# Kernel tuning notes

Hardware: AMD Instinct MI355X
Metric: run time of the kernel (lower is better)

## Reference

```python
import jax, jax.numpy as jnp
import numpy as np

B, V, C, D, H, W = 2, 3, 32, 48, 128, 160


def _bilinear_sample(img, x, y):
    # img: [C,H,W]; x,y: [N] pixel coords; zero padding outside the image
    Ci, Hi, Wi = img.shape
    x0 = jnp.floor(x); y0 = jnp.floor(y)
    x1 = x0 + 1.0; y1 = y0 + 1.0
    wx1 = x - x0; wx0 = 1.0 - wx1
    wy1 = y - y0; wy0 = 1.0 - wy1

    def gather(xi, yi):
        valid = (xi >= 0) & (xi <= Wi - 1) & (yi >= 0) & (yi <= Hi - 1)
        xc = jnp.clip(xi, 0, Wi - 1).astype(jnp.int32)
        yc = jnp.clip(yi, 0, Hi - 1).astype(jnp.int32)
        return img[:, yc, xc] * valid.astype(img.dtype)  # [C,N]

    return (gather(x0, y0) * (wx0 * wy0) + gather(x1, y0) * (wx1 * wy0)
            + gather(x0, y1) * (wx0 * wy1) + gather(x1, y1) * (wx1 * wy1))


def homo_warping(src_fea, src_proj, ref_proj, depth_values):
    # src_fea [B,C,H,W], projs [B,4,4], depth_values [B,D] -> [B,C,D,H,W]
    Bn, Cn, Hn, Wn = src_fea.shape
    Dn = depth_values.shape[1]
    proj = src_proj @ jnp.linalg.inv(ref_proj)          # [B,4,4]
    rot = proj[:, :3, :3]
    trans = proj[:, :3, 3]
    ys, xs = jnp.meshgrid(jnp.arange(Hn, dtype=src_fea.dtype),
                          jnp.arange(Wn, dtype=src_fea.dtype), indexing='ij')
    xyz = jnp.stack([xs.ravel(), ys.ravel(), jnp.ones(Hn * Wn, src_fea.dtype)])  # [3,HW]
    rot_xyz = jnp.einsum('bij,jn->bin', rot, xyz)       # [B,3,HW]
    pts = rot_xyz[:, :, None, :] * depth_values[:, None, :, None] \
          + trans[:, :, None, None]                     # [B,3,D,HW]
    z = pts[:, 2]
    z = jnp.where(jnp.abs(z) < 1e-6, 1e-6, z)
    px = (pts[:, 0] / z).reshape(Bn, -1)                # [B,D*HW]
    py = (pts[:, 1] / z).reshape(Bn, -1)
    warped = jax.vmap(_bilinear_sample)(src_fea, px, py)  # [B,C,D*HW]
    return warped.reshape(Bn, Cn, Dn, Hn, Wn)


def setup_inputs():
    key = jax.random.key(0)
    k1, k2 = jax.random.split(key)
    features = jax.random.normal(k1, (V, B, C, H, W), jnp.float32)
    # realistic pinhole projection matrices K @ [R|t] (4x4)
    f = 300.0
    K = np.array([[f, 0, W / 2, 0], [0, f, H / 2, 0],
                  [0, 0, 1, 0], [0, 0, 0, 1]], np.float32)
    projs = []
    for v in range(V):
        E = np.eye(4, dtype=np.float32)
        E[0, 3] = 2.0 * v   # small camera baseline
        E[1, 3] = -1.0 * v
        projs.append(K @ E)
    proj_matrices = jnp.asarray(np.broadcast_to(np.stack(projs), (B, V, 4, 4)).copy())
    depth_values = jnp.tile(jnp.linspace(425.0, 935.0, D, dtype=jnp.float32)[None], (B, 1))
    reg_w = jax.random.normal(k2, (1, C, 3, 3, 3), jnp.float32) * 0.05
    reg_b = jnp.zeros((1,), jnp.float32)
    return {"features": features, "proj_matrices": proj_matrices,
            "depth_values": depth_values, "num_depth": D,
            "reg_w": reg_w, "reg_b": reg_b}


def reference(features, proj_matrices, depth_values, num_depth, reg_w, reg_b):
    num_views = features.shape[0]
    ref_feature = features[0]                         # [B,C,H,W]
    ref_proj = proj_matrices[:, 0]
    Bn, Cn, Hn, Wn = ref_feature.shape
    ref_volume = jnp.broadcast_to(ref_feature[:, :, None], (Bn, Cn, num_depth, Hn, Wn))
    volume_sum = ref_volume
    volume_sq_sum = ref_volume ** 2
    for v in range(1, num_views):
        wv = homo_warping(features[v], proj_matrices[:, v], ref_proj, depth_values)
        volume_sum = volume_sum + wv
        volume_sq_sum = volume_sq_sum + wv * wv
    variance = volume_sq_sum / num_views - (volume_sum / num_views) ** 2
    # cost regularization: Conv3d(C->1, k=3, pad=1)
    cost = jax.lax.conv_general_dilated(
        variance, reg_w, (1, 1, 1), [(1, 1), (1, 1), (1, 1)],
        dimension_numbers=('NCDHW', 'OIDHW', 'NCDHW'))
    cost = cost + reg_b[None, :, None, None, None]
    prob = jax.nn.softmax(cost[:, 0], axis=1)         # [B,D,H,W]
    depth = jnp.sum(prob * depth_values[:, :, None, None], axis=1)  # [B,H,W]
    # photometric confidence: sum over 4 consecutive depth probs (== 4*avg_pool3d)
    psum4 = jax.lax.reduce_window(prob, 0.0, jax.lax.add, (1, 4, 1, 1), (1, 1, 1, 1),
                                  [(0, 0), (1, 2), (0, 0), (0, 0)])
    didx = jnp.sum(prob * jnp.arange(num_depth, dtype=prob.dtype)[None, :, None, None], axis=1)
    didx = jnp.clip(didx.astype(jnp.int32), 0, num_depth - 1)
    conf = jnp.take_along_axis(psum4, didx[:, None], axis=1)[:, 0]
    return depth, conf
```

## Files before the change

### kernel.cpp

```cpp
#include <hip/hip_runtime.h>
#include <hip/hip_bf16.h>
#include <hip/hip_fp16.h>

#define Hh 128
#define Ww 160
#define Cc 32
#define Dd 48
#define Bb 2
#define Vv 3
#define HW (Hh*Ww)
#define VS 32

typedef _Float16 f16x8 __attribute__((ext_vector_type(8)));
typedef float f32x4 __attribute__((ext_vector_type(4)));

__global__ void k_transpose(const float* __restrict__ f, const float* __restrict__ pm,
                            const float* __restrict__ wt, ushort* __restrict__ featT,
                            float* __restrict__ P, ushort* __restrict__ Bfr) {
    __shared__ float t[Cc][Ww + 1];
    const int tid = threadIdx.x;
    if (blockIdx.x == 0 && tid < 64) {
        if (tid < Bb * (Vv - 1)) {
            int b = tid >> 1;
            int v = (tid & 1) + 1;
            const float* ref = pm + (b * Vv + 0) * 16;
            const float* src = pm + (b * Vv + v) * 16;
            float A[4][8];
            for (int i = 0; i < 4; ++i)
                for (int j = 0; j < 4; ++j) {
                    A[i][j] = ref[i * 4 + j];
                    A[i][4 + j] = (i == j) ? 1.0f : 0.0f;
                }
            for (int col = 0; col < 4; ++col) {
                int piv = col;
                for (int r = col + 1; r < 4; ++r)
                    if (fabsf(A[r][col]) > fabsf(A[piv][col])) piv = r;
                if (piv != col)
                    for (int j = 0; j < 8; ++j) { float tmp = A[col][j]; A[col][j] = A[piv][j]; A[piv][j] = tmp; }
                float inv = 1.0f / A[col][col];
                for (int j = 0; j < 8; ++j) A[col][j] *= inv;
                for (int r = 0; r < 4; ++r) {
                    if (r == col) continue;
                    float fct = A[r][col];
                    for (int j = 0; j < 8; ++j) A[r][j] -= fct * A[col][j];
                }
            }
            float Pm[3][4];
            for (int i = 0; i < 3; ++i)
                for (int j = 0; j < 4; ++j) {
                    float s = 0.f;
                    for (int k = 0; k < 4; ++k) s += src[i * 4 + k] * A[k][4 + j];
                    Pm[i][j] = s;
                }
            float* o = P + tid * 12;
            o[0] = Pm[0][0]; o[1] = Pm[0][1]; o[2] = Pm[0][2];
            o[3] = Pm[1][0]; o[4] = Pm[1][1]; o[5] = Pm[1][2];
            o[6] = Pm[2][0]; o[7] = Pm[2][1]; o[8] = Pm[2][2];
            o[9] = Pm[0][3]; o[10] = Pm[1][3]; o[11] = Pm[2][3];
        }
        int kd = tid & 15, q = tid >> 4;
        for (int tap = 0; tap < 9; ++tap) {
            ushort* dst = Bfr + (tap * 64 + tid) * 8;
            for (int j = 0; j < 8; ++j) {
                float w = (kd < 3) ? wt[(q * 8 + j) * 27 + kd * 9 + tap] : 0.f;
                __half h = __float2half(w);
                dst[j] = *(ushort*)&h;
            }
        }
    }
    int slice = blockIdx.x;
    int vb = slice / Hh, y = slice % Hh;
    const float* src = f + (size_t)vb * Cc * HW + (size_t)y * Ww;
    ushort* dst = featT + ((size_t)vb * Hh + y) * Ww * Cc;
    for (int i = tid; i < Cc * (Ww / 4); i += 256) {
        int c = i / (Ww / 4), x4 = (i - c * (Ww / 4)) * 4;
        float4 v = *(const float4*)(src + (size_t)c * HW + x4);
        t[c][x4] = v.x; t[c][x4 + 1] = v.y; t[c][x4 + 2] = v.z; t[c][x4 + 3] = v.w;
    }
    __syncthreads();
    for (int i = tid; i < Ww * 4; i += 256) {
        int x = i >> 2, c8 = i & 3;
        union { uint4 u; ushort s[8]; } pk;
#pragma unroll
        for (int j = 0; j < 8; ++j) {
            __half h = __float2half(t[c8 * 8 + j][x]);
            pk.s[j] = *(ushort*)&h;
        }
        *(uint4*)&dst[x * Cc + c8 * 8] = pk.u;
    }
}

__global__ __launch_bounds__(256, 4)
void k_main(const ushort* __restrict__ featT, const float* __restrict__ P,
            const float* __restrict__ dvals, const ushort* __restrict__ Bfr,
            ushort* __restrict__ S) {
    __shared__ ushort vsh[324 * VS];
    __shared__ unsigned int offs[324 * 8];
    __shared__ unsigned int wgts[324 * 4];
    __shared__ float rt[24];
    const int tid = threadIdx.x;
    const int b = blockIdx.z, d = blockIdx.y;
    const int tileY = blockIdx.x / 10, tileX = blockIdx.x - (blockIdx.x / 10) * 10;

    if (tid < 24) rt[tid] = P[b * 24 + tid];
    const float depth = dvals[b * Dd + d];
    __syncthreads();

#pragma unroll 1
    for (int p = tid; p < 324; p += 256) {
        int pyt = p / 18, pxt = p - pyt * 18;
        int gy = tileY * 16 + pyt - 1, gx = tileX * 16 + pxt - 1;
        if ((unsigned)gy >= (unsigned)Hh || (unsigned)gx >= (unsigned)Ww) continue;
#pragma unroll
        for (int vi = 0; vi < 2; ++vi) {
            const float* M = &rt[vi * 12];
            float fgx = (float)gx, fgy = (float)gy;
            float rx = M[0] * fgx + M[1] * fgy + M[2];
            float ry = M[3] * fgx + M[4] * fgy + M[5];
            float rz = M[6] * fgx + M[7] * fgy + M[8];
            float X = rx * depth + M[9];
            float Y = ry * depth + M[10];
            float Z = rz * depth + M[11];
            float z = (fabsf(Z) < 1e-6f) ? 1e-6f : Z;
            float u = X / z, vv = Y / z;
            float x0f = floorf(u), y0f = floorf(vv);
            float fx = u - x0f, fy = vv - y0f;
            int x0 = (int)x0f, y0 = (int)y0f;
            int x1 = x0 + 1, y1 = y0 + 1;
            bool vx0 = (x0 >= 0) && (x0 <= Ww - 1);
            bool vx1 = (x1 >= 0) && (x1 <= Ww - 1);
            bool vy0 = (y0 >= 0) && (y0 <= Hh - 1);
            bool vy1 = (y1 >= 0) && (y1 <= Hh - 1);
            int xc0 = min(max(x0, 0), Ww - 1), xc1 = min(max(x1, 0), Ww - 1);
            int yc0 = min(max(y0, 0), Hh - 1), yc1 = min(max(y1, 0), Hh - 1);
            unsigned int p00 = (unsigned)(yc0 * Ww + xc0);
            unsigned int p01 = (unsigned)(yc0 * Ww + xc1);
            unsigned int p10 = (unsigned)(yc1 * Ww + xc0);
            unsigned int p11 = (unsigned)(yc1 * Ww + xc1);
            float w0 = (vx0 && vy0) ? (1.f - fx) * (1.f - fy) : 0.f;
            float w1 = (vx1 && vy0) ? fx * (1.f - fy) : 0.f;
            float w2 = (vx0 && vy1) ? (1.f - fx) * fy : 0.f;
            float w3 = (vx1 && vy1) ? fx * fy : 0.f;
            unsigned int* od = &offs[p * 8 + vi * 4];
            od[0] = p00 << 6;
            od[1] = p01 << 6;
            od[2] = p10 << 6;
            od[3] = p11 << 6;
            __half2 ha = __floats2half2_rn(w0, w1);
            __half2 hb = __floats2half2_rn(w2, w3);
            wgts[p * 4 + vi * 2 + 0] = *(unsigned int*)&ha;
            wgts[p * 4 + vi * 2 + 1] = *(unsigned int*)&hb;
        }
    }
    __syncthreads();

    const ushort* b1 = featT + (size_t)(1 * Bb + b) * HW * Cc;
    const ushort* b2 = featT + (size_t)(2 * Bb + b) * HW * Cc;
    const ushort* br = featT + (size_t)b * HW * Cc;

#pragma unroll 1
    for (int i = tid; i < 1296; i += 256) {
        int p = i >> 2, q = i & 3;
        int pyt = p / 18, pxt = p - pyt * 18;
        int gy = tileY * 16 + pyt - 1, gx = tileX * 16 + pxt - 1;
        ushort* dst = &vsh[p * VS + ((q ^ (p & 3)) << 3)];
        if ((unsigned)gy >= (unsigned)Hh || (unsigned)gx >= (unsigned)Ww) {
            *(uint4*)dst = make_uint4(0u, 0u, 0u, 0u);
            continue;
        }
        const unsigned int qb = (unsigned)(q << 4);
        const uint4 o1 = *(const uint4*)&offs[p * 8];
        const uint4 o2 = *(const uint4*)&offs[p * 8 + 4];
        const uint4 wwp = *(const uint4*)&wgts[p * 4];
        __half2 hv0 = *(__half2*)&wwp.x;
        __half2 hv1 = *(__half2*)&wwp.y;
        __half2 hv2 = *(__half2*)&wwp.z;
        __half2 hv3 = *(__half2*)&wwp.w;
        __half2 w00 = __half2half2(__low2half(hv0)), w01 = __half2half2(__high2half(hv0));
        __half2 w02 = __half2half2(__low2half(hv1)), w03 = __half2half2(__high2half(hv1));
        __half2 w10 = __half2half2(__low2half(hv2)), w11 = __half2half2(__high2half(hv2));
        __half2 w12 = __half2half2(__low2half(hv3)), w13 = __half2half2(__high2half(hv3));
        const __half2 third2 = __float2half2_rn(1.0f / 3.0f);
        union U { uint4 u; __half2 h[4]; };
        U R_, C0, C1, C2, C3, E0, E1, E2, E3, V;
        R_.u = *(const uint4*)((const char*)br + ((unsigned)((gy * Ww + gx) << 6) + qb));
        C0.u = *(const uint4*)((const char*)b1 + (o1.x + qb));
        C1.u = *(const uint4*)((const char*)b1 + (o1.y + qb));
        C2.u = *(const uint4*)((const char*)b1 + (o1.z + qb));
        C3.u = *(const uint4*)((const char*)b1 + (o1.w + qb));
        E0.u = *(const uint4*)((const char*)b2 + (o2.x + qb));
        E1.u = *(const uint4*)((const char*)b2 + (o2.y + qb));
        E2.u = *(const uint4*)((const char*)b2 + (o2.z + qb));
        E3.u = *(const uint4*)((const char*)b2 + (o2.w + qb));
#pragma unroll
        for (int k = 0; k < 4; ++k) {
            __half2 s1 = __hmul2(w00, C0.h[k]);
            s1 = __hfma2(w01, C1.h[k], s1);
            s1 = __hfma2(w02, C2.h[k], s1);
            s1 = __hfma2(w03, C3.h[k], s1);
            __half2 s2 = __hmul2(w10, E0.h[k]);
            s2 = __hfma2(w11, E1.h[k], s2);
            s2 = __hfma2(w12, E2.h[k], s2);
            s2 = __hfma2(w13, E3.h[k], s2);
            __half2 r = R_.h[k];
            __half2 sum = __hadd2(__hadd2(r, s1), s2);
            __half2 sq = __hmul2(r, r);
            sq = __hfma2(s1, s1, sq);
            sq = __hfma2(s2, s2, sq);
            __half2 m = __hmul2(sum, third2);
            __half2 var = __hfma2(__hneg2(m), m, __hmul2(sq, third2));
            V.h[k] = var;
        }
        *(uint4*)dst = V.u;
    }
    __syncthreads();

    const int lane = tid & 63;
    const int wave = tid >> 6;
    const int q = lane >> 4;
    const int n = lane & 15;
    uint4 bf[9];
#pragma unroll
    for (int tap = 0; tap < 9; ++tap)
        bf[tap] = *(const uint4*)(Bfr + ((tap * 64 + lane) << 3));
#pragma unroll 1
    for (int rr = 0; rr < 4; ++rr) {
        int row = wave * 4 + rr;
        f32x4 acc = {0.f, 0.f, 0.f, 0.f};
#pragma unroll
        for (int tap = 0; tap < 9; ++tap) {
            int kh = tap / 3, kw = tap - 3 * (tap / 3);
            int slot = (row + kh) * 18 + n + kw;
            union { uint4 u; f16x8 v; } A, Bf;
            A.u  = *(const uint4*)&vsh[slot * VS + (q ^ (slot & 3)) * 8];
            Bf.u = bf[tap];
            acc = __builtin_amdgcn_mfma_f32_16x16x32_f16(A.v, Bf.v, acc, 0, 0, 0);
        }
        if (n < 3) {
            int gy = tileY * 16 + row;
            int gxb = tileX * 16 + q * 4;
            union { uint2 u; ushort s[4]; } pk;
#pragma unroll
            for (int j = 0; j < 4; ++j) {
                __half h = __float2half(acc[j]);
                pk.s[j] = *(ushort*)&h;
            }
            *(uint2*)&S[((size_t)(b * 3 + n) * Dd + d) * HW + (size_t)gy * Ww + gxb] = pk.u;
        }
    }
}

__global__ __launch_bounds__(256)
void k_post(const ushort* __restrict__ S, const float* __restrict__ dvals,
            float* __restrict__ out) {
    const int tid = threadIdx.x;
    const int lane = tid & 63, wave = tid >> 6;
    const int q = lane >> 4;
    const int pl = lane & 15;
    int gid = ((blockIdx.x * 4 + wave) * 16 + pl) * 2;
    int b = gid / HW;
    int pix = gid - b * HW;
    const ushort* S0 = S + ((size_t)(b * 3 + 0) * Dd) * HW + pix;
    const ushort* S1 = S + ((size_t)(b * 3 + 1) * Dd) * HW + pix;
    const ushort* S2 = S + ((size_t)(b * 3 + 2) * Dd) * HW + pix;
    const int d0 = q * 12;
    float2 cost[12];
#pragma unroll
    for (int j = 0; j < 12; ++j) {
        int dd = d0 + j;
        float2 c = __half22float2(*(const __half2*)&S1[(size_t)dd * HW]);
        if (dd > 0) {
            float2 a = __half22float2(*(const __half2*)&S0[(size_t)(dd - 1) * HW]);
            c.x += a.x; c.y += a.y;
        }
        if (dd < Dd - 1) {
            float2 a = __half22float2(*(const __half2*)&S2[(size_t)(dd + 1) * HW]);
            c.x += a.x; c.y += a.y;
        }
        cost[j] = c;
    }
    float mx = cost[0].x, my = cost[0].y;
#pragma unroll
    for (int j = 1; j < 12; ++j) { mx = fmaxf(mx, cost[j].x); my = fmaxf(my, cost[j].y); }
    mx = fmaxf(mx, __shfl_xor(mx, 16)); mx = fmaxf(mx, __shfl_xor(mx, 32));
    my = fmaxf(my, __shfl_xor(my, 16)); my = fmaxf(my, __shfl_xor(my, 32));
    float sx = 0.f, sy = 0.f, depx = 0.f, depy = 0.f, dix = 0.f, diy = 0.f;
#pragma unroll
    for (int j = 0; j < 12; ++j) {
        float dv = dvals[b * Dd + d0 + j];
        float fd = (float)(d0 + j);
        float ex = __expf(cost[j].x - mx);
        float ey = __expf(cost[j].y - my);
        cost[j].x = ex; cost[j].y = ey;
        sx += ex; sy += ey;
        depx += ex * dv; depy += ey * dv;
        dix += ex * fd;  diy += ey * fd;
    }
    sx += __shfl_xor(sx, 16); sx += __shfl_xor(sx, 32);
    sy += __shfl_xor(sy, 16); sy += __shfl_xor(sy, 32);
    depx += __shfl_xor(depx, 16); depx += __shfl_xor(depx, 32);
    depy += __shfl_xor(depy, 16); depy += __shfl_xor(depy, 32);
    dix += __shfl_xor(dix, 16); dix += __shfl_xor(dix, 32);
    diy += __shfl_xor(diy, 16); diy += __shfl_xor(diy, 32);
    float invx = 1.0f / sx, invy = 1.0f / sy;
    int didx = min(max((int)(dix * invx), 0), Dd - 1);
    int didy = min(max((int)(diy * invy), 0), Dd - 1);
    float wx = 0.f, wy = 0.f;
#pragma unroll
    for (int j = 0; j < 12; ++j) {
        int dd = d0 + j;
        wx += ((dd >= didx - 1) && (dd <= didx + 2)) ? cost[j].x : 0.f;
        wy += ((dd >= didy - 1) && (dd <= didy + 2)) ? cost[j].y : 0.f;
    }
    wx += __shfl_xor(wx, 16); wx += __shfl_xor(wx, 32);
    wy += __shfl_xor(wy, 16); wy += __shfl_xor(wy, 32);
    if (q == 0) {
        *(float2*)&out[gid] = make_float2(depx * invx, depy * invy);
        *(float2*)&out[Bb * HW + gid] = make_float2(wx * invx, wy * invy);
    }
}

extern "C" void kernel_launch(void* const* d_in, const int* in_sizes, int n_in,
                              void* d_out, int out_size, void* d_ws, size_t ws_size,
                              hipStream_t stream) {
    const float* features = (const float*)d_in[0];
    const float* pm       = (const float*)d_in[1];
    const float* dvals    = (const float*)d_in[2];
    const float* reg_w    = (const float*)d_in[4];
    float* outp = (float*)d_out;

    char* ws = (char*)d_ws;
    ushort* featT = (ushort*)ws;
    size_t featT_bytes = (size_t)Vv * Bb * Hh * Ww * Cc * sizeof(ushort);
    float* P = (float*)(ws + featT_bytes);
    ushort* S = (ushort*)(ws + featT_bytes + 512);
    size_t S_bytes = (size_t)Bb * 3 * Dd * HW * sizeof(ushort);
    ushort* Bfr = (ushort*)(ws + featT_bytes + 512 + S_bytes);

    k_transpose<<<Vv * Bb * Hh, 256, 0, stream>>>(features, pm, reg_w, featT, P, Bfr);
    k_main<<<dim3(80, Dd, Bb), 256, 0, stream>>>(featT, P, dvals, Bfr, S);
    k_post<<<(Bb * HW) / 128, 256, 0, stream>>>(S, dvals, outp);
}
```

Measured before the change: 153.5 us.

## Fuse variance into MFMA: apply per-tap channel weights then spatially sum in LDS

```diff
diff --git a/kernel.cpp b/kernel.cpp
--- a/kernel.cpp
+++ b/kernel.cpp
@@ -9,7 +9,7 @@
 #define Bb 2
 #define Vv 3
 #define HW (Hh*Ww)
-#define VS 32
+#define TSTRIDE 340
 
 typedef _Float16 f16x8 __attribute__((ext_vector_type(8)));
 typedef float f32x4 __attribute__((ext_vector_type(4)));
@@ -58,13 +58,16 @@
             o[6] = Pm[2][0]; o[7] = Pm[2][1]; o[8] = Pm[2][2];
             o[9] = Pm[0][3]; o[10] = Pm[1][3]; o[11] = Pm[2][3];
         }
-        int kd = tid & 15, q = tid >> 4;
-        for (int tap = 0; tap < 9; ++tap) {
-            ushort* dst = Bfr + (tap * 64 + tid) * 8;
-            for (int j = 0; j < 8; ++j) {
-                float w = (kd < 3) ? wt[(q * 8 + j) * 27 + kd * 9 + tap] : 0.f;
+        int j16 = tid & 15, q = tid >> 4;
+        for (int m = 0; m < 3; ++m) {
+            ushort* dst = Bfr + (m * 64 + tid) * 8;
+            int j = m * 16 + j16;
+            int tap = j >> 2, kd = j & 3;
+            bool valid = (tap < 9) && (kd < 3);
+            for (int e = 0; e < 8; ++e) {
+                float w = valid ? wt[(q * 8 + e) * 27 + kd * 9 + tap] : 0.f;
                 __half h = __float2half(w);
-                dst[j] = *(ushort*)&h;
+                dst[e] = *(ushort*)&h;
             }
         }
     }
@@ -94,9 +97,9 @@
 void k_main(const ushort* __restrict__ featT, const float* __restrict__ P,
             const float* __restrict__ dvals, const ushort* __restrict__ Bfr,
             ushort* __restrict__ S) {
-    __shared__ ushort vsh[324 * VS];
-    __shared__ unsigned int offs[324 * 8];
+    __shared__ unsigned int offs[324 * 4];
     __shared__ unsigned int wgts[324 * 4];
+    __shared__ ushort t2[36 * TSTRIDE];
     __shared__ float rt[24];
     const int tid = threadIdx.x;
     const int b = blockIdx.z, d = blockIdx.y;
@@ -141,11 +144,8 @@
             float w1 = (vx1 && vy0) ? fx * (1.f - fy) : 0.f;
             float w2 = (vx0 && vy1) ? (1.f - fx) * fy : 0.f;
             float w3 = (vx1 && vy1) ? fx * fy : 0.f;
-            unsigned int* od = &offs[p * 8 + vi * 4];
-            od[0] = p00 << 6;
-            od[1] = p01 << 6;
-            od[2] = p10 << 6;
-            od[3] = p11 << 6;
+            offs[p * 4 + vi * 2 + 0] = p00 | (p01 << 16);
+            offs[p * 4 + vi * 2 + 1] = p10 | (p11 << 16);
             __half2 ha = __floats2half2_rn(w0, w1);
             __half2 hb = __floats2half2_rn(w2, w3);
             wgts[p * 4 + vi * 2 + 0] = *(unsigned int*)&ha;
@@ -158,95 +158,122 @@
     const ushort* b2 = featT + (size_t)(2 * Bb + b) * HW * Cc;
     const ushort* br = featT + (size_t)b * HW * Cc;
 
-#pragma unroll 1
-    for (int i = tid; i < 1296; i += 256) {
-        int p = i >> 2, q = i & 3;
-        int pyt = p / 18, pxt = p - pyt * 18;
-        int gy = tileY * 16 + pyt - 1, gx = tileX * 16 + pxt - 1;
-        ushort* dst = &vsh[p * VS + ((q ^ (p & 3)) << 3)];
-        if ((unsigned)gy >= (unsigned)Hh || (unsigned)gx >= (unsigned)Ww) {
-            *(uint4*)dst = make_uint4(0u, 0u, 0u, 0u);
-            continue;
-        }
-        const unsigned int qb = (unsigned)(q << 4);
-        const uint4 o1 = *(const uint4*)&offs[p * 8];
-        const uint4 o2 = *(const uint4*)&offs[p * 8 + 4];
-        const uint4 wwp = *(const uint4*)&wgts[p * 4];
-        __half2 hv0 = *(__half2*)&wwp.x;
-        __half2 hv1 = *(__half2*)&wwp.y;
-        __half2 hv2 = *(__half2*)&wwp.z;
-        __half2 hv3 = *(__half2*)&wwp.w;
-        __half2 w00 = __half2half2(__low2half(hv0)), w01 = __half2half2(__high2half(hv0));
-        __half2 w02 = __half2half2(__low2half(hv1)), w03 = __half2half2(__high2half(hv1));
-        __half2 w10 = __half2half2(__low2half(hv2)), w11 = __half2half2(__high2half(hv2));
-        __half2 w12 = __half2half2(__low2half(hv3)), w13 = __half2half2(__high2half(hv3));
-        const __half2 third2 = __float2half2_rn(1.0f / 3.0f);
-        union U { uint4 u; __half2 h[4]; };
-        U R_, C0, C1, C2, C3, E0, E1, E2, E3, V;
-        R_.u = *(const uint4*)((const char*)br + ((unsigned)((gy * Ww + gx) << 6) + qb));
-        C0.u = *(const uint4*)((const char*)b1 + (o1.x + qb));
-        C1.u = *(const uint4*)((const char*)b1 + (o1.y + qb));
-        C2.u = *(const uint4*)((const char*)b1 + (o1.z + qb));
-        C3.u = *(const uint4*)((const char*)b1 + (o1.w + qb));
-        E0.u = *(const uint4*)((const char*)b2 + (o2.x + qb));
-        E1.u = *(const uint4*)((const char*)b2 + (o2.y + qb));
-        E2.u = *(const uint4*)((const char*)b2 + (o2.z + qb));
-        E3.u = *(const uint4*)((const char*)b2 + (o2.w + qb));
-#pragma unroll
-        for (int k = 0; k < 4; ++k) {
-            __half2 s1 = __hmul2(w00, C0.h[k]);
-            s1 = __hfma2(w01, C1.h[k], s1);
-            s1 = __hfma2(w02, C2.h[k], s1);
-            s1 = __hfma2(w03, C3.h[k], s1);
-            __half2 s2 = __hmul2(w10, E0.h[k]);
-            s2 = __hfma2(w11, E1.h[k], s2);
-            s2 = __hfma2(w12, E2.h[k], s2);
-            s2 = __hfma2(w13, E3.h[k], s2);
-            __half2 r = R_.h[k];
-            __half2 sum = __hadd2(__hadd2(r, s1), s2);
-            __half2 sq = __hmul2(r, r);
-            sq = __hfma2(s1, s1, sq);
-            sq = __hfma2(s2, s2, sq);
-            __half2 m = __hmul2(sum, third2);
-            __half2 var = __hfma2(__hneg2(m), m, __hmul2(sq, third2));
-            V.h[k] = var;
-        }
-        *(uint4*)dst = V.u;
-    }
-    __syncthreads();
-
     const int lane = tid & 63;
     const int wave = tid >> 6;
     const int q = lane >> 4;
     const int n = lane & 15;
-    uint4 bf[9];
-#pragma unroll
-    for (int tap = 0; tap < 9; ++tap)
-        bf[tap] = *(const uint4*)(Bfr + ((tap * 64 + lane) << 3));
+
+    union F { uint4 u; __half2 h[4]; f16x8 v; };
+    F Bf0, Bf1, Bf2;
+    Bf0.u = *(const uint4*)(Bfr + (0 * 64 + lane) * 8);
+    Bf1.u = *(const uint4*)(Bfr + (1 * 64 + lane) * 8);
+    Bf2.u = *(const uint4*)(Bfr + (2 * 64 + lane) * 8);
+
 #pragma unroll 1
-    for (int rr = 0; rr < 4; ++rr) {
-        int row = wave * 4 + rr;
-        f32x4 acc = {0.f, 0.f, 0.f, 0.f};
-#pragma unroll
-        for (int tap = 0; tap < 9; ++tap) {
-            int kh = tap / 3, kw = tap - 3 * (tap / 3);
-            int slot = (row + kh) * 18 + n + kw;
-            union { uint4 u; f16x8 v; } A, Bf;
-            A.u  = *(const uint4*)&vsh[slot * VS + (q ^ (slot & 3)) * 8];
-            Bf.u = bf[tap];
-            acc = __builtin_amdgcn_mfma_f32_16x16x32_f16(A.v, Bf.v, acc, 0, 0, 0);
-        }
-        if (n < 3) {
-            int gy = tileY * 16 + row;
-            int gxb = tileX * 16 + q * 4;
-            union { uint2 u; ushort s[4]; } pk;
-#pragma unroll
-            for (int j = 0; j < 4; ++j) {
-                __half h = __float2half(acc[j]);
-                pk.s[j] = *(ushort*)&h;
+    for (int g = wave; g < 21; g += 4) {
+        int slot = g * 16 + n;
+        int p = (slot < 324) ? slot : 323;
+        int pyt = p / 18, pxt = p - pyt * 18;
+        int gy = tileY * 16 + pyt - 1, gx = tileX * 16 + pxt - 1;
+        bool live = (slot < 324) && ((unsigned)gy < (unsigned)Hh) && ((unsigned)gx < (unsigned)Ww);
+        F V;
+        V.u = make_uint4(0u, 0u, 0u, 0u);
+        if (live) {
+            const unsigned qb = (unsigned)(q << 4);
+            uint4 oo = *(const uint4*)&offs[p * 4];
+            uint4 wwp = *(const uint4*)&wgts[p * 4];
+            const char* b1c = (const char*)b1 + qb;
+            const char* b2c = (const char*)b2 + qb;
+            unsigned o00 = (oo.x & 0xffffu) << 6;
+            unsigned o01 = (oo.x >> 16) << 6;
+            unsigned o10 = (oo.y & 0xffffu) << 6;
+            unsigned o11 = (oo.y >> 16) << 6;
+            unsigned o20 = (oo.z & 0xffffu) << 6;
+            unsigned o21 = (oo.z >> 16) << 6;
+            unsigned o30 = (oo.w & 0xffffu) << 6;
+            unsigned o31 = (oo.w >> 16) << 6;
+            __half2 hv0 = *(__half2*)&wwp.x;
+            __half2 hv1 = *(__half2*)&wwp.y;
+            __half2 hv2 = *(__half2*)&wwp.z;
+            __half2 hv3 = *(__half2*)&wwp.w;
+            __half2 w00 = __half2half2(__low2half(hv0)), w01 = __half2half2(__high2half(hv0));
+            __half2 w02 = __half2half2(__low2half(hv1)), w03 = __half2half2(__high2half(hv1));
+            __half2 w10 = __half2half2(__low2half(hv2)), w11 = __half2half2(__high2half(hv2));
+            __half2 w12 = __half2half2(__low2half(hv3)), w13 = __half2half2(__high2half(hv3));
+            const __half2 third2 = __float2half2_rn(1.0f / 3.0f);
+            F R_, C0, C1, C2, C3, E0, E1, E2, E3;
+            R_.u = *(const uint4*)((const char*)br + (((unsigned)(gy * Ww + gx)) << 6) + qb);
+            C0.u = *(const uint4*)(b1c + o00);
+            C1.u = *(const uint4*)(b1c + o01);
+            C2.u = *(const uint4*)(b1c + o10);
+            C3.u = *(const uint4*)(b1c + o11);
+            E0.u = *(const uint4*)(b2c + o20);
+            E1.u = *(const uint4*)(b2c + o21);
+            E2.u = *(const uint4*)(b2c + o30);
+            E3.u = *(const uint4*)(b2c + o31);
+#pragma unroll
+            for (int k = 0; k < 4; ++k) {
+                __half2 s1 = __hmul2(w00, C0.h[k]);
+                s1 = __hfma2(w01, C1.h[k], s1);
+                s1 = __hfma2(w02, C2.h[k], s1);
+                s1 = __hfma2(w03, C3.h[k], s1);
+                __half2 s2 = __hmul2(w10, E0.h[k]);
+                s2 = __hfma2(w11, E1.h[k], s2);
+                s2 = __hfma2(w12, E2.h[k], s2);
+                s2 = __hfma2(w13, E3.h[k], s2);
+                __half2 r = R_.h[k];
+                __half2 sum = __hadd2(__hadd2(r, s1), s2);
+                __half2 sq = __hmul2(r, r);
+                sq = __hfma2(s1, s1, sq);
+                sq = __hfma2(s2, s2, sq);
+                __half2 m = __hmul2(sum, third2);
+                __half2 var = __hfma2(__hneg2(m), m, __hmul2(sq, third2));
+                V.h[k] = var;
             }
-            *(uint2*)&S[((size_t)(b * 3 + n) * Dd + d) * HW + (size_t)gy * Ww + gxb] = pk.u;
-        }
+        }
+        f32x4 a0 = {0.f, 0.f, 0.f, 0.f};
+        f32x4 a1 = {0.f, 0.f, 0.f, 0.f};
+        f32x4 a2 = {0.f, 0.f, 0.f, 0.f};
+        a0 = __builtin_amdgcn_mfma_f32_16x16x32_f16(V.v, Bf0.v, a0, 0, 0, 0);
+        a1 = __builtin_amdgcn_mfma_f32_16x16x32_f16(V.v, Bf1.v, a1, 0, 0, 0);
+        a2 = __builtin_amdgcn_mfma_f32_16x16x32_f16(V.v, Bf2.v, a2, 0, 0, 0);
+        int sb = g * 16 + q * 4;
+        union { uint2 u; ushort s[4]; } pk;
+#pragma unroll
+        for (int r = 0; r < 4; ++r) { __half h = __float2half(a0[r]); pk.s[r] = *(ushort*)&h; }
+        *(uint2*)&t2[(0 * 16 + n) * TSTRIDE + sb] = pk.u;
+#pragma unroll
+        for (int r = 0; r < 4; ++r) { __half h = __float2half(a1[r]); pk.s[r] = *(ushort*)&h; }
+        *(uint2*)&t2[(16 + n) * TSTRIDE + sb] = pk.u;
+        if (n < 4) {
+#pragma unroll
+            for (int r = 0; r < 4; ++r) { __half h = __float2half(a2[r]); pk.s[r] = *(ushort*)&h; }
+            *(uint2*)&t2[(32 + n) * TSTRIDE + sb] = pk.u;
+        }
+    }
+    __syncthreads();
+
+    {
+        int x = tid & 15, y = tid >> 4;
+        float s0 = 0.f, s1 = 0.f, s2 = 0.f;
+#pragma unroll
+        for (int ky = 0; ky < 3; ++ky) {
+#pragma unroll
+            for (int kx = 0; kx < 3; ++kx) {
+                int tap = ky * 3 + kx;
+                int sl = (y + ky) * 18 + (x + kx);
+                const ushort* tp = &t2[(tap * 4) * TSTRIDE + sl];
+                s0 += __half2float(*(const __half*)&tp[0]);
+                s1 += __half2float(*(const __half*)&tp[TSTRIDE]);
+                s2 += __half2float(*(const __half*)&tp[2 * TSTRIDE]);
+            }
+        }
+        int gy = tileY * 16 + y, gx = tileX * 16 + x;
+        size_t base = (size_t)gy * Ww + gx;
+        __half h0 = __float2half(s0), h1 = __float2half(s1), h2 = __float2half(s2);
+        S[((size_t)(b * 3 + 0) * Dd + d) * HW + base] = *(ushort*)&h0;
+        S[((size_t)(b * 3 + 1) * Dd + d) * HW + base] = *(ushort*)&h1;
+        S[((size_t)(b * 3 + 2) * Dd + d) * HW + base] = *(ushort*)&h2;
     }
 }
 
```

Result: slower. 170.2 us (+10.9%).

## Stage source-view bounding windows in LDS and loop over depth chunks per block

Applied to the files above, without the earlier changes.

```diff
diff --git a/kernel.cpp b/kernel.cpp
--- a/kernel.cpp
+++ b/kernel.cpp
@@ -10,6 +10,9 @@
 #define Vv 3
 #define HW (Hh*Ww)
 #define VS 32
+#define WPX 336
+#define NSLOT 180
+#define DCH 16
 
 typedef _Float16 f16x8 __attribute__((ext_vector_type(8)));
 typedef float f32x4 __attribute__((ext_vector_type(4)));
@@ -90,67 +93,75 @@
     }
 }
 
-__global__ __launch_bounds__(256, 4)
+__global__ __launch_bounds__(256, 2)
 void k_main(const ushort* __restrict__ featT, const float* __restrict__ P,
             const float* __restrict__ dvals, const ushort* __restrict__ Bfr,
             ushort* __restrict__ S) {
-    __shared__ ushort vsh[324 * VS];
-    __shared__ unsigned int offs[324 * 8];
-    __shared__ unsigned int wgts[324 * 4];
+    __shared__ ushort win[2 * WPX * 32];
+    __shared__ ushort refw[NSLOT * 32];
+    __shared__ ushort vsh[NSLOT * VS];
+    __shared__ unsigned int offs[NSLOT * 4];
+    __shared__ unsigned int wgts[NSLOT * 4];
     __shared__ float rt[24];
+    __shared__ float uvz[2][8][3];
+    __shared__ int bb[8];
+    __shared__ int wok[2];
     const int tid = threadIdx.x;
-    const int b = blockIdx.z, d = blockIdx.y;
+    const int b = blockIdx.z;
+    const int cb = blockIdx.y * DCH;
     const int tileY = blockIdx.x / 10, tileX = blockIdx.x - (blockIdx.x / 10) * 10;
 
     if (tid < 24) rt[tid] = P[b * 24 + tid];
-    const float depth = dvals[b * Dd + d];
     __syncthreads();
 
-#pragma unroll 1
-    for (int p = tid; p < 324; p += 256) {
-        int pyt = p / 18, pxt = p - pyt * 18;
-        int gy = tileY * 16 + pyt - 1, gx = tileX * 16 + pxt - 1;
-        if ((unsigned)gy >= (unsigned)Hh || (unsigned)gx >= (unsigned)Ww) continue;
-#pragma unroll
-        for (int vi = 0; vi < 2; ++vi) {
-            const float* M = &rt[vi * 12];
-            float fgx = (float)gx, fgy = (float)gy;
-            float rx = M[0] * fgx + M[1] * fgy + M[2];
-            float ry = M[3] * fgx + M[4] * fgy + M[5];
-            float rz = M[6] * fgx + M[7] * fgy + M[8];
-            float X = rx * depth + M[9];
-            float Y = ry * depth + M[10];
-            float Z = rz * depth + M[11];
-            float z = (fabsf(Z) < 1e-6f) ? 1e-6f : Z;
-            float u = X / z, vv = Y / z;
-            float x0f = floorf(u), y0f = floorf(vv);
-            float fx = u - x0f, fy = vv - y0f;
-            int x0 = (int)x0f, y0 = (int)y0f;
-            int x1 = x0 + 1, y1 = y0 + 1;
-            bool vx0 = (x0 >= 0) && (x0 <= Ww - 1);
-            bool vx1 = (x1 >= 0) && (x1 <= Ww - 1);
-            bool vy0 = (y0 >= 0) && (y0 <= Hh - 1);
-            bool vy1 = (y1 >= 0) && (y1 <= Hh - 1);
-            int xc0 = min(max(x0, 0), Ww - 1), xc1 = min(max(x1, 0), Ww - 1);
-            int yc0 = min(max(y0, 0), Hh - 1), yc1 = min(max(y1, 0), Hh - 1);
-            unsigned int p00 = (unsigned)(yc0 * Ww + xc0);
-            unsigned int p01 = (unsigned)(yc0 * Ww + xc1);
-            unsigned int p10 = (unsigned)(yc1 * Ww + xc0);
-            unsigned int p11 = (unsigned)(yc1 * Ww + xc1);
-            float w0 = (vx0 && vy0) ? (1.f - fx) * (1.f - fy) : 0.f;
-            float w1 = (vx1 && vy0) ? fx * (1.f - fy) : 0.f;
-            float w2 = (vx0 && vy1) ? (1.f - fx) * fy : 0.f;
-            float w3 = (vx1 && vy1) ? fx * fy : 0.f;
-            unsigned int* od = &offs[p * 8 + vi * 4];
-            od[0] = p00 << 6;
-            od[1] = p01 << 6;
-            od[2] = p10 << 6;
-            od[3] = p11 << 6;
-            __half2 ha = __floats2half2_rn(w0, w1);
-            __half2 hb = __floats2half2_rn(w2, w3);
-            wgts[p * 4 + vi * 2 + 0] = *(unsigned int*)&ha;
-            wgts[p * 4 + vi * 2 + 1] = *(unsigned int*)&hb;
-        }
+    if (tid < 16) {
+        int vi = tid >> 3, s = tid & 7;
+        int corner = s & 3, de = s >> 2;
+        float dmn = 1e30f, dmx = -1e30f;
+        for (int k = 0; k < DCH; ++k) {
+            float dv = dvals[b * Dd + cb + k];
+            dmn = fminf(dmn, dv); dmx = fmaxf(dmx, dv);
+        }
+        float depth = de ? dmx : dmn;
+        float fgx = (float)(tileX * 16 + ((corner & 1) ? 16 : -1));
+        float fgy = (float)(tileY * 8 + ((corner & 2) ? 8 : -1));
+        const float* M = &rt[vi * 12];
+        float rx = M[0] * fgx + M[1] * fgy + M[2];
+        float ry = M[3] * fgx + M[4] * fgy + M[5];
+        float rz = M[6] * fgx + M[7] * fgy + M[8];
+        float X = rx * depth + M[9];
+        float Y = ry * depth + M[10];
+        float Z = rz * depth + M[11];
+        float z = (fabsf(Z) < 1e-6f) ? 1e-6f : Z;
+        uvz[vi][s][0] = X / z;
+        uvz[vi][s][1] = Y / z;
+        uvz[vi][s][2] = Z;
+    }
+    __syncthreads();
+    if (tid < 2) {
+        int vi = tid;
+        float umin = 1e30f, umax = -1e30f, vmin = 1e30f, vmax = -1e30f;
+        int npos = 0, nneg = 0;
+        for (int s = 0; s < 8; ++s) {
+            float u = uvz[vi][s][0], v = uvz[vi][s][1], z = uvz[vi][s][2];
+            npos += (z > 1e-5f); nneg += (z < -1e-5f);
+            umin = fminf(umin, u); umax = fmaxf(umax, u);
+            vmin = fminf(vmin, v); vmax = fmaxf(vmax, v);
+        }
+        bool ok = (npos == 8) || (nneg == 8);
+        ok = ok && (umin <= umax) && (vmin <= vmax);
+        umin = fmaxf(fminf(umin, 1e5f), -1e5f); umax = fmaxf(fminf(umax, 1e5f), -1e5f);
+        vmin = fmaxf(fminf(vmin, 1e5f), -1e5f); vmax = fmaxf(fminf(vmax, 1e5f), -1e5f);
+        int bx = max(0, (int)floorf(umin) - 1);
+        int ex = min(Ww - 1, (int)ceilf(umax) + 2);
+        int by = max(0, (int)floorf(vmin) - 1);
+        int ey = min(Hh - 1, (int)ceilf(vmax) + 2);
+        int ww2 = ex - bx + 1, wh2 = ey - by + 1;
+        ok = ok && (ww2 > 0) && (wh2 > 0) && (ww2 * wh2 <= WPX);
+        if (!ok) { bx = 0; by = 0; ww2 = 1; wh2 = 1; }
+        bb[vi * 4 + 0] = bx; bb[vi * 4 + 1] = by;
+        bb[vi * 4 + 2] = ww2; bb[vi * 4 + 3] = wh2;
+        wok[vi] = ok ? 1 : 0;
     }
     __syncthreads();
 
@@ -158,95 +169,205 @@
     const ushort* b2 = featT + (size_t)(2 * Bb + b) * HW * Cc;
     const ushort* br = featT + (size_t)b * HW * Cc;
 
-#pragma unroll 1
-    for (int i = tid; i < 1296; i += 256) {
-        int p = i >> 2, q = i & 3;
+#pragma unroll
+    for (int vi = 0; vi < 2; ++vi) {
+        if (!wok[vi]) continue;
+        int bx = bb[vi * 4 + 0], by = bb[vi * 4 + 1], ww2 = bb[vi * 4 + 2], wh2 = bb[vi * 4 + 3];
+        const ushort* src = vi ? b2 : b1;
+        ushort* wdst = win + vi * (WPX * 32);
+        int total = ww2 * wh2 * 4;
+        for (int i = tid; i < total; i += 256) {
+            int q = i & 3, w = i >> 2;
+            int wy = w / ww2, wx = w - wy * ww2;
+            *(uint4*)&wdst[(w << 5) + (q << 3)] =
+                *(const uint4*)&src[(size_t)((by + wy) * Ww + bx + wx) * Cc + (q << 3)];
+        }
+    }
+    for (int i = tid; i < NSLOT * 4; i += 256) {
+        int q = i & 3, p = i >> 2;
         int pyt = p / 18, pxt = p - pyt * 18;
-        int gy = tileY * 16 + pyt - 1, gx = tileX * 16 + pxt - 1;
-        ushort* dst = &vsh[p * VS + ((q ^ (p & 3)) << 3)];
-        if ((unsigned)gy >= (unsigned)Hh || (unsigned)gx >= (unsigned)Ww) {
-            *(uint4*)dst = make_uint4(0u, 0u, 0u, 0u);
-            continue;
-        }
-        const unsigned int qb = (unsigned)(q << 4);
-        const uint4 o1 = *(const uint4*)&offs[p * 8];
-        const uint4 o2 = *(const uint4*)&offs[p * 8 + 4];
-        const uint4 wwp = *(const uint4*)&wgts[p * 4];
-        __half2 hv0 = *(__half2*)&wwp.x;
-        __half2 hv1 = *(__half2*)&wwp.y;
-        __half2 hv2 = *(__half2*)&wwp.z;
-        __half2 hv3 = *(__half2*)&wwp.w;
-        __half2 w00 = __half2half2(__low2half(hv0)), w01 = __half2half2(__high2half(hv0));
-        __half2 w02 = __half2half2(__low2half(hv1)), w03 = __half2half2(__high2half(hv1));
-        __half2 w10 = __half2half2(__low2half(hv2)), w11 = __half2half2(__high2half(hv2));
-        __half2 w12 = __half2half2(__low2half(hv3)), w13 = __half2half2(__high2half(hv3));
-        const __half2 third2 = __float2half2_rn(1.0f / 3.0f);
-        union U { uint4 u; __half2 h[4]; };
-        U R_, C0, C1, C2, C3, E0, E1, E2, E3, V;
-        R_.u = *(const uint4*)((const char*)br + ((unsigned)((gy * Ww + gx) << 6) + qb));
-        C0.u = *(const uint4*)((const char*)b1 + (o1.x + qb));
-        C1.u = *(const uint4*)((const char*)b1 + (o1.y + qb));
-        C2.u = *(const uint4*)((const char*)b1 + (o1.z + qb));
-        C3.u = *(const uint4*)((const char*)b1 + (o1.w + qb));
-        E0.u = *(const uint4*)((const char*)b2 + (o2.x + qb));
-        E1.u = *(const uint4*)((const char*)b2 + (o2.y + qb));
-        E2.u = *(const uint4*)((const char*)b2 + (o2.z + qb));
-        E3.u = *(const uint4*)((const char*)b2 + (o2.w + qb));
-#pragma unroll
-        for (int k = 0; k < 4; ++k) {
-            __half2 s1 = __hmul2(w00, C0.h[k]);
-            s1 = __hfma2(w01, C1.h[k], s1);
-            s1 = __hfma2(w02, C2.h[k], s1);
-            s1 = __hfma2(w03, C3.h[k], s1);
-            __half2 s2 = __hmul2(w10, E0.h[k]);
-            s2 = __hfma2(w11, E1.h[k], s2);
-            s2 = __hfma2(w12, E2.h[k], s2);
-            s2 = __hfma2(w13, E3.h[k], s2);
-            __half2 r = R_.h[k];
-            __half2 sum = __hadd2(__hadd2(r, s1), s2);
-            __half2 sq = __hmul2(r, r);
-            sq = __hfma2(s1, s1, sq);
-            sq = __hfma2(s2, s2, sq);
-            __half2 m = __hmul2(sum, third2);
-            __half2 var = __hfma2(__hneg2(m), m, __hmul2(sq, third2));
-            V.h[k] = var;
-        }
-        *(uint4*)dst = V.u;
-    }
-    __syncthreads();
+        int gy = tileY * 8 + pyt - 1, gx = tileX * 16 + pxt - 1;
+        if ((unsigned)gy < (unsigned)Hh && (unsigned)gx < (unsigned)Ww)
+            *(uint4*)&refw[(p << 5) + (q << 3)] =
+                *(const uint4*)&br[(size_t)(gy * Ww + gx) * Cc + (q << 3)];
+    }
 
     const int lane = tid & 63;
     const int wave = tid >> 6;
-    const int q = lane >> 4;
-    const int n = lane & 15;
+    const int q2 = lane >> 4;
+    const int n2 = lane & 15;
     uint4 bf[9];
 #pragma unroll
     for (int tap = 0; tap < 9; ++tap)
         bf[tap] = *(const uint4*)(Bfr + ((tap * 64 + lane) << 3));
+
+    const int bx0 = bb[0], by0 = bb[1], ww0 = bb[2], wh0 = bb[3];
+    const int bx1 = bb[4], by1 = bb[5], ww1 = bb[6], wh1 = bb[7];
+    const int wk0 = wok[0], wk1 = wok[1];
+    __syncthreads();
+
 #pragma unroll 1
-    for (int rr = 0; rr < 4; ++rr) {
-        int row = wave * 4 + rr;
-        f32x4 acc = {0.f, 0.f, 0.f, 0.f};
-#pragma unroll
-        for (int tap = 0; tap < 9; ++tap) {
-            int kh = tap / 3, kw = tap - 3 * (tap / 3);
-            int slot = (row + kh) * 18 + n + kw;
-            union { uint4 u; f16x8 v; } A, Bf;
-            A.u  = *(const uint4*)&vsh[slot * VS + (q ^ (slot & 3)) * 8];
-            Bf.u = bf[tap];
-            acc = __builtin_amdgcn_mfma_f32_16x16x32_f16(A.v, Bf.v, acc, 0, 0, 0);
-        }
-        if (n < 3) {
-            int gy = tileY * 16 + row;
-            int gxb = tileX * 16 + q * 4;
-            union { uint2 u; ushort s[4]; } pk;
-#pragma unroll
-            for (int j = 0; j < 4; ++j) {
-                __half h = __float2half(acc[j]);
-                pk.s[j] = *(ushort*)&h;
-            }
-            *(uint2*)&S[((size_t)(b * 3 + n) * Dd + d) * HW + (size_t)gy * Ww + gxb] = pk.u;
-        }
+    for (int dd = 0; dd < DCH; ++dd) {
+        const int d = cb + dd;
+        const float depth = dvals[b * Dd + d];
+
+#pragma unroll 1
+        for (int p = tid; p < NSLOT; p += 256) {
+            int pyt = p / 18, pxt = p - pyt * 18;
+            int gy = tileY * 8 + pyt - 1, gx = tileX * 16 + pxt - 1;
+            if ((unsigned)gy >= (unsigned)Hh || (unsigned)gx >= (unsigned)Ww) continue;
+#pragma unroll
+            for (int vi = 0; vi < 2; ++vi) {
+                const float* M = &rt[vi * 12];
+                float fgx = (float)gx, fgy = (float)gy;
+                float rx = M[0] * fgx + M[1] * fgy + M[2];
+                float ry = M[3] * fgx + M[4] * fgy + M[5];
+                float rz = M[6] * fgx + M[7] * fgy + M[8];
+                float X = rx * depth + M[9];
+                float Y = ry * depth + M[10];
+                float Z = rz * depth + M[11];
+                float z = (fabsf(Z) < 1e-6f) ? 1e-6f : Z;
+                float u = X / z, vv = Y / z;
+                float x0f = floorf(u), y0f = floorf(vv);
+                float fx = u - x0f, fy = vv - y0f;
+                int x0 = (int)x0f, y0 = (int)y0f;
+                int x1 = x0 + 1, y1 = y0 + 1;
+                bool vx0 = (x0 >= 0) && (x0 <= Ww - 1);
+                bool vx1 = (x1 >= 0) && (x1 <= Ww - 1);
+                bool vy0 = (y0 >= 0) && (y0 <= Hh - 1);
+                bool vy1 = (y1 >= 0) && (y1 <= Hh - 1);
+                int xc0 = min(max(x0, 0), Ww - 1), xc1 = min(max(x1, 0), Ww - 1);
+                int yc0 = min(max(y0, 0), Hh - 1), yc1 = min(max(y1, 0), Hh - 1);
+                float w0 = (vx0 && vy0) ? (1.f - fx) * (1.f - fy) : 0.f;
+                float w1 = (vx1 && vy0) ? fx * (1.f - fy) : 0.f;
+                float w2 = (vx0 && vy1) ? (1.f - fx) * fy : 0.f;
+                float w3 = (vx1 && vy1) ? fx * fy : 0.f;
+                int bx = vi ? bx1 : bx0, by = vi ? by1 : by0;
+                int ww2 = vi ? ww1 : ww0, wh2 = vi ? wh1 : wh0;
+                int wk = vi ? wk1 : wk0;
+                bool allin = wk && (xc0 >= bx) && (xc1 <= bx + ww2 - 1)
+                                && (yc0 >= by) && (yc1 <= by + wh2 - 1);
+                unsigned i00, i01, i10, i11;
+                if (allin) {
+                    int ry0 = (yc0 - by) * ww2, ry1 = (yc1 - by) * ww2;
+                    i00 = (unsigned)(ry0 + xc0 - bx);
+                    i01 = (unsigned)(ry0 + xc1 - bx);
+                    i10 = (unsigned)(ry1 + xc0 - bx);
+                    i11 = (unsigned)(ry1 + xc1 - bx);
+                } else {
+                    i00 = 0x8000u | (unsigned)(yc0 * Ww + xc0);
+                    i01 = 0x8000u | (unsigned)(yc0 * Ww + xc1);
+                    i10 = 0x8000u | (unsigned)(yc1 * Ww + xc0);
+                    i11 = 0x8000u | (unsigned)(yc1 * Ww + xc1);
+                }
+                offs[p * 4 + vi * 2 + 0] = i00 | (i01 << 16);
+                offs[p * 4 + vi * 2 + 1] = i10 | (i11 << 16);
+                __half2 ha = __floats2half2_rn(w0, w1);
+                __half2 hb = __floats2half2_rn(w2, w3);
+                wgts[p * 4 + vi * 2 + 0] = *(unsigned int*)&ha;
+                wgts[p * 4 + vi * 2 + 1] = *(unsigned int*)&hb;
+            }
+        }
+        __syncthreads();
+
+#pragma unroll 1
+        for (int i = tid; i < NSLOT * 4; i += 256) {
+            int p = i >> 2, q = i & 3;
+            int pyt = p / 18, pxt = p - pyt * 18;
+            int gy = tileY * 8 + pyt - 1, gx = tileX * 16 + pxt - 1;
+            ushort* dst = &vsh[p * VS + ((q ^ (p & 3)) << 3)];
+            if ((unsigned)gy >= (unsigned)Hh || (unsigned)gx >= (unsigned)Ww) {
+                *(uint4*)dst = make_uint4(0u, 0u, 0u, 0u);
+                continue;
+            }
+            const int qb = q << 3;
+            uint4 oo = *(const uint4*)&offs[p * 4];
+            uint4 wwp = *(const uint4*)&wgts[p * 4];
+            union U { uint4 u; __half2 h[4]; };
+            U R_, C0, C1, C2, C3, E0, E1, E2, E3, V;
+            R_.u = *(const uint4*)&refw[(p << 5) + qb];
+            if (!((oo.x | oo.y) & 0x80008000u)) {
+                const ushort* w0p = win;
+                C0.u = *(const uint4*)&w0p[((oo.x & 0xffffu) << 5) + qb];
+                C1.u = *(const uint4*)&w0p[((oo.x >> 16) << 5) + qb];
+                C2.u = *(const uint4*)&w0p[((oo.y & 0xffffu) << 5) + qb];
+                C3.u = *(const uint4*)&w0p[((oo.y >> 16) << 5) + qb];
+            } else {
+                C0.u = *(const uint4*)&b1[(size_t)(oo.x & 0x7fffu) * Cc + qb];
+                C1.u = *(const uint4*)&b1[(size_t)((oo.x >> 16) & 0x7fffu) * Cc + qb];
+                C2.u = *(const uint4*)&b1[(size_t)(oo.y & 0x7fffu) * Cc + qb];
+                C3.u = *(const uint4*)&b1[(size_t)((oo.y >> 16) & 0x7fffu) * Cc + qb];
+            }
+            if (!((oo.z | oo.w) & 0x80008000u)) {
+                const ushort* w1p = win + WPX * 32;
+                E0.u = *(const uint4*)&w1p[((oo.z & 0xffffu) << 5) + qb];
+                E1.u = *(const uint4*)&w1p[((oo.z >> 16) << 5) + qb];
+                E2.u = *(const uint4*)&w1p[((oo.w & 0xffffu) << 5) + qb];
+                E3.u = *(const uint4*)&w1p[((oo.w >> 16) << 5) + qb];
+            } else {
+                E0.u = *(const uint4*)&b2[(size_t)(oo.z & 0x7fffu) * Cc + qb];
+                E1.u = *(const uint4*)&b2[(size_t)((oo.z >> 16) & 0x7fffu) * Cc + qb];
+                E2.u = *(const uint4*)&b2[(size_t)(oo.w & 0x7fffu) * Cc + qb];
+                E3.u = *(const uint4*)&b2[(size_t)((oo.w >> 16) & 0x7fffu) * Cc + qb];
+            }
+            __half2 hv0 = *(__half2*)&wwp.x;
+            __half2 hv1 = *(__half2*)&wwp.y;
+            __half2 hv2 = *(__half2*)&wwp.z;
+            __half2 hv3 = *(__half2*)&wwp.w;
+            __half2 w00 = __half2half2(__low2half(hv0)), w01 = __half2half2(__high2half(hv0));
+            __half2 w02 = __half2half2(__low2half(hv1)), w03 = __half2half2(__high2half(hv1));
+            __half2 w10 = __half2half2(__low2half(hv2)), w11 = __half2half2(__high2half(hv2));
+            __half2 w12 = __half2half2(__low2half(hv3)), w13 = __half2half2(__high2half(hv3));
+            const __half2 third2 = __float2half2_rn(1.0f / 3.0f);
+#pragma unroll
+            for (int k = 0; k < 4; ++k) {
+                __half2 s1 = __hmul2(w00, C0.h[k]);
+                s1 = __hfma2(w01, C1.h[k], s1);
+                s1 = __hfma2(w02, C2.h[k], s1);
+                s1 = __hfma2(w03, C3.h[k], s1);
+                __half2 s2 = __hmul2(w10, E0.h[k]);
+                s2 = __hfma2(w11, E1.h[k], s2);
+                s2 = __hfma2(w12, E2.h[k], s2);
+                s2 = __hfma2(w13, E3.h[k], s2);
+                __half2 r = R_.h[k];
+                __half2 sum = __hadd2(__hadd2(r, s1), s2);
+                __half2 sq = __hmul2(r, r);
+                sq = __hfma2(s1, s1, sq);
+                sq = __hfma2(s2, s2, sq);
+                __half2 m = __hmul2(sum, third2);
+                __half2 var = __hfma2(__hneg2(m), m, __hmul2(sq, third2));
+                V.h[k] = var;
+            }
+            *(uint4*)dst = V.u;
+        }
+        __syncthreads();
+
+#pragma unroll 1
+        for (int rr = 0; rr < 2; ++rr) {
+            int row = wave * 2 + rr;
+            f32x4 acc = {0.f, 0.f, 0.f, 0.f};
+#pragma unroll
+            for (int tap = 0; tap < 9; ++tap) {
+                int kh = tap / 3, kw = tap - 3 * (tap / 3);
+                int slot = (row + kh) * 18 + n2 + kw;
+                union { uint4 u; f16x8 v; } A, Bf;
+                A.u = *(const uint4*)&vsh[slot * VS + (q2 ^ (slot & 3)) * 8];
+                Bf.u = bf[tap];
+                acc = __builtin_amdgcn_mfma_f32_16x16x32_f16(A.v, Bf.v, acc, 0, 0, 0);
+            }
+            if (n2 < 3) {
+                int gy = tileY * 8 + row;
+                int gxb = tileX * 16 + q2 * 4;
+                union { uint2 u; ushort s[4]; } pk;
+#pragma unroll
+                for (int j = 0; j < 4; ++j) {
+                    __half h = __float2half(acc[j]);
+                    pk.s[j] = *(ushort*)&h;
+                }
+                *(uint2*)&S[((size_t)(b * 3 + n2) * Dd + d) * HW + (size_t)gy * Ww + gxb] = pk.u;
+            }
+        }
+        __syncthreads();
     }
 }
 
@@ -338,6 +459,6 @@
     ushort* Bfr = (ushort*)(ws + featT_bytes + 512 + S_bytes);
 
     k_transpose<<<Vv * Bb * Hh, 256, 0, stream>>>(features, pm, reg_w, featT, P, Bfr);
-    k_main<<<dim3(80, Dd, Bb), 256, 0, stream>>>(featT, P, dvals, Bfr, S);
+    k_main<<<dim3(160, Dd / DCH, Bb), 256, 0, stream>>>(featT, P, dvals, Bfr, S);
     k_post<<<(Bb * HW) / 128, 256, 0, stream>>>(S, dvals, outp);
 }
```

Result: slower. 205.8 us (+34.1%).
